# Kernel tuning notes

Hardware: AMD Instinct MI355X
Metric: run time of the kernel (lower is better)

The kernel has to match this reference:

```python
import jax, jax.numpy as jnp
import numpy as np

RADII = [2, 4]
EPS = 1e-6


def _avg_pool_hw(t, k):
    # valid avg-pool with kernel k, stride 1 over the last two dims
    nd = t.ndim
    win = (1,) * (nd - 2) + (k, k)
    s = jax.lax.reduce_window(t, 0.0, jax.lax.add, win, (1,) * nd, 'VALID')
    return s / float(k * k)


def _patch_cca(x, y, r):
    B, C1, H, W = x.shape
    C2 = y.shape[1]
    k = 2 * r + 1
    pad = ((0, 0), (0, 0), (r, r), (r, r))
    xp = jnp.pad(x, pad, mode='reflect')  # (B,C1,Hp,Wp)
    yp = jnp.pad(y, pad, mode='reflect')  # (B,C2,Hp,Wp)

    # local second moments via outer products + avg pooling
    xx = _avg_pool_hw(xp[:, :, None] * xp[:, None], k)  # (B,C1,C1,H,W)
    yy = _avg_pool_hw(yp[:, :, None] * yp[:, None], k)  # (B,C2,C2,H,W)
    xy = _avg_pool_hw(xp[:, :, None] * yp[:, None], k)  # (B,C1,C2,H,W)
    xm = _avg_pool_hw(xp, k)  # (B,C1,H,W)
    ym = _avg_pool_hw(yp, k)  # (B,C2,H,W)

    cxx = xx - xm[:, :, None] * xm[:, None]
    cyy = yy - ym[:, :, None] * ym[:, None]
    cxy = xy - xm[:, :, None] * ym[:, None]

    # move matrix dims last: (B,H,W,Ci,Cj)
    cxx = jnp.transpose(cxx, (0, 3, 4, 1, 2)) + EPS * jnp.eye(C1, dtype=x.dtype)
    cyy = jnp.transpose(cyy, (0, 3, 4, 1, 2)) + EPS * jnp.eye(C2, dtype=x.dtype)
    cxy = jnp.transpose(cxy, (0, 3, 4, 1, 2))

    lx_inv = jnp.linalg.inv(jnp.linalg.cholesky(cxx))  # (B,H,W,C1,C1)
    ly_inv = jnp.linalg.inv(jnp.linalg.cholesky(cyy))  # (B,H,W,C2,C2)
    corr = jnp.einsum('bhwij,bhwjk,bhwkl->bhwil', lx_inv, cxy, ly_inv)
    diag = jnp.diagonal(corr, axis1=-2, axis2=-1)  # (B,H,W,min(C1,C2))
    sim = jnp.abs(diag).sum(-1) / min(C1, C2)  # (B,H,W)
    return sim[:, None]  # (B,1,H,W)


def setup_inputs() -> dict:
    key = jax.random.key(0)
    kx, ky = jax.random.split(key)
    B, C, H, W = 2, 6, 512, 512
    x = jax.random.normal(kx, (B, C, H, W), dtype=jnp.float32)
    y = jax.random.normal(ky, (B, C, H, W), dtype=jnp.float32)
    return {'x': x, 'y': y}


def reference(x, y):
    # stack per-radius CCA maps on a trailing axis -> (B,1,H,W,len(RADII))
    return jnp.stack([_patch_cca(x, y, r) for r in RADII], axis=-1)
```

## Files before the change

kernel.cpp:

```cpp
#include <hip/hip_runtime.h>
#include <math.h>

typedef float v2f __attribute__((ext_vector_type(2)));
typedef float v4f __attribute__((ext_vector_type(4)));

#define LT(i,j) ((i)*((i)+1)/2 + (j))

__device__ __forceinline__ int reflect512(int i) {
  int a = (i < 0) ? -i : i;
  int b = 1022 - a;
  return (a < b) ? a : b;
}

constexpr int HB  = 520;
constexpr int PS  = 12;
constexpr int RS  = HB * PS;

__global__ __launch_bounds__(256)
void prep_interleave(const float* __restrict__ xg, const float* __restrict__ yg,
                     float* __restrict__ zb) {
  constexpr int H = 512, W = 512, HW = H * W;
  const int idx = blockIdx.x * 256 + threadIdx.x;
  if (idx >= 2 * HB * HB) return;
  const int b  = idx / (HB * HB);
  const int r2 = idx - b * (HB * HB);
  const int hr = r2 / HB;
  const int wc = r2 - hr * HB;
  const int h = reflect512(hr - 4);
  const int w = reflect512(wc - 4);
  const size_t gp = (size_t)b * 6 * HW + (size_t)h * W + w;
  float xv[6], yv[6];
  #pragma unroll
  for (int c = 0; c < 6; ++c) {
    xv[c] = xg[gp + c * HW];
    yv[c] = yg[gp + c * HW];
  }
  float* o = zb + (size_t)idx * PS;
  v4f p0 = {xv[0], xv[1], xv[2], xv[3]};
  v4f p1 = {xv[4], xv[5], yv[0], yv[1]};
  v4f p2 = {yv[2], yv[3], yv[4], yv[5]};
  *(v4f*)(o + 0) = p0;
  *(v4f*)(o + 4) = p1;
  *(v4f*)(o + 8) = p2;
}

__device__ __forceinline__ float gget(const v2f* accd, const v2f* accs,
                                      int a, int b) {
  const int t = LT(a >> 1, b >> 1);
  if (((a & 1) == 0) && ((b & 1) == 0)) return accd[t].x;
  if (((a & 1) == 1) && ((b & 1) == 1)) return accd[t].y;
  if ((a & 1) == 0) return accs[t].x;
  return accs[t].y;
}

__device__ __forceinline__ void cholinv6(float* a) {
  #pragma unroll
  for (int j = 0; j < 6; ++j) {
    float d = a[LT(j,j)];
    #pragma unroll
    for (int p = 0; p < j; ++p) d -= a[LT(j,p)] * a[LT(j,p)];
    const float rd = __builtin_amdgcn_rsqf(d);
    a[LT(j,j)] = rd;
    #pragma unroll
    for (int i = j + 1; i < 6; ++i) {
      float s = a[LT(i,j)];
      #pragma unroll
      for (int p = 0; p < j; ++p) s -= a[LT(i,p)] * a[LT(j,p)];
      a[LT(i,j)] = s * rd;
    }
  }
  #pragma unroll
  for (int j = 0; j < 6; ++j) {
    #pragma unroll
    for (int i = j + 1; i < 6; ++i) {
      float s = 0.0f;
      #pragma unroll
      for (int p = j; p < i; ++p) s += a[LT(i,p)] * a[LT(p,j)];
      a[LT(i,j)] = -s * a[LT(i,i)];
    }
  }
}

template <int K, bool ADD>
__device__ __forceinline__ void row_acc_g(const float* __restrict__ p,
                                          v2f* zs, v2f* accd, v2f* accs) {
  #pragma unroll
  for (int dx = 0; dx < K; ++dx) {
    const v4f l0 = *(const v4f*)(p + dx * PS + 0);
    const v4f l1 = *(const v4f*)(p + dx * PS + 4);
    const v4f l2 = *(const v4f*)(p + dx * PS + 8);
    v2f z[6];
    z[0] = l0.lo; z[1] = l0.hi;
    z[2] = l1.lo; z[3] = l1.hi;
    z[4] = l2.lo; z[5] = l2.hi;
    #pragma unroll
    for (int q = 0; q < 6; ++q) zs[q] = ADD ? (zs[q] + z[q]) : (zs[q] - z[q]);
    int t = 0;
    #pragma unroll
    for (int Kp = 0; Kp < 6; ++Kp) {
      #pragma unroll
      for (int Pp = 0; Pp <= Kp; ++Pp) {
        const v2f c  = z[Pp];
        const v2f cs = __builtin_shufflevector(c, c, 1, 0);
        const v2f a  = ADD ? z[Kp] : -z[Kp];
        accd[t] = __builtin_elementwise_fma(a, c,  accd[t]);
        accs[t] = __builtin_elementwise_fma(a, cs, accs[t]);
        ++t;
      }
    }
  }
}

template <int K>
__device__ __forceinline__ float emit_sim(const v2f* zs, const v2f* accd,
                                          const v2f* accs) {
  constexpr float inv_n = 1.0f / (K * K);
  float mx[6], my[6];
  #pragma unroll
  for (int i = 0; i < 6; ++i) {
    mx[i] = ((i & 1) ? zs[i >> 1].y : zs[i >> 1].x) * inv_n;
    my[i] = ((i & 1) ? zs[3 + (i >> 1)].y : zs[3 + (i >> 1)].x) * inv_n;
  }
  float ax[21];
  {
    int t = 0;
    #pragma unroll
    for (int i = 0; i < 6; ++i)
      #pragma unroll
      for (int j = 0; j <= i; ++j) {
        const float e = (i == j) ? 1e-6f : 0.0f;
        ax[t] = gget(accd, accs, i, j) * inv_n - mx[i] * mx[j] + e;
        ++t;
      }
  }
  cholinv6(ax);
  float ay[21];
  {
    int t = 0;
    #pragma unroll
    for (int i = 0; i < 6; ++i)
      #pragma unroll
      for (int j = 0; j <= i; ++j) {
        const float e = (i == j) ? 1e-6f : 0.0f;
        ay[t] = gget(accd, accs, 6 + i, 6 + j) * inv_n - my[i] * my[j] + e;
        ++t;
      }
  }
  cholinv6(ay);
  float cxy[36];
  #pragma unroll
  for (int i = 0; i < 6; ++i)
    #pragma unroll
    for (int j = 0; j < 6; ++j)
      cxy[i * 6 + j] = fmaf(-mx[i], my[j], gget(accd, accs, 6 + j, i) * inv_n);
  float sim = 0.0f;
  #pragma unroll
  for (int i = 0; i < 6; ++i) {
    float di = 0.0f;
    #pragma unroll
    for (int j = 0; j <= i; ++j) {
      float inner = 0.0f;
      #pragma unroll
      for (int k = i; k < 6; ++k) inner += cxy[j * 6 + k] * ay[LT(k, i)];
      di += ax[LT(i, j)] * inner;
    }
    sim += fabsf(di);
  }
  return sim * (1.0f / 6.0f);
}

template <int R, int V>
__device__ __forceinline__ void run(const float* __restrict__ zb,
                                    float* __restrict__ out, int b, int ri) {
  constexpr int K = 2 * R + 1;
  constexpr int H = 512, W = 512;

  const int h0 = blockIdx.y * (16 * V);
  const int w0 = blockIdx.x * 16;
  const int tx = threadIdx.x & 15;
  const int g  = threadIdx.x >> 4;
  const int hbase = h0 + g * V;
  const int wc = w0 + tx;

  const float* base = zb + (size_t)b * HB * RS
                    + (size_t)(hbase + 4 - R) * RS + (size_t)(wc + 4 - R) * PS;

  v2f zs[6]    = {};
  v2f accd[21] = {};
  v2f accs[21] = {};

  #pragma unroll 1
  for (int dy = 0; dy < K; ++dy)
    row_acc_g<K, true>(base + dy * RS, zs, accd, accs);

  out[((size_t)((b * H + hbase) * W + wc)) * 2 + ri] =
      emit_sim<K>(zs, accd, accs);

  #pragma unroll 1
  for (int s = 1; s < V; ++s) {
    row_acc_g<K, true >(base + (s + 2 * R) * RS, zs, accd, accs);
    row_acc_g<K, false>(base + (s - 1)     * RS, zs, accd, accs);
    out[((size_t)((b * H + hbase + s) * W + wc)) * 2 + ri] =
        emit_sim<K>(zs, accd, accs);
  }
}

__global__ __launch_bounds__(256, 2)
void cca_v8(const float* __restrict__ zb, float* __restrict__ out) {
  const int z = blockIdx.z;
  if (z < 2) run<2, 8>(zb, out, z, 0);
  else       run<4, 8>(zb, out, z - 2, 1);
}

extern "C" void kernel_launch(void* const* d_in, const int* in_sizes, int n_in,
                              void* d_out, int out_size, void* d_ws, size_t ws_size,
                              hipStream_t stream) {
  const float* x = (const float*)d_in[0];
  const float* y = (const float*)d_in[1];
  float* out = (float*)d_out;
  float* zb  = (float*)d_ws;

  {
    const int n = 2 * HB * HB;
    prep_interleave<<<dim3((n + 255) / 256), dim3(256), 0, stream>>>(x, y, zb);
  }
  dim3 grid(512 / 16, 512 / (16 * 8), 4);
  cca_v8<<<grid, dim3(256), 0, stream>>>(zb, out);
}
```

Before: 138.7 us.

## Vectorize prep interleave and rebalance radius work across grid blocks

The prep kernel now has each thread handle four consecutive columns. Interior threads use 128-bit loads, and only the reflected border uses scalar loads. The main kernel grid is rebuilt so the heavier radius-4 path runs with 4 rows per thread over more blocks, while the radius-2 path keeps 8 rows per thread. This is meant to even out per-block work and cut tail imbalance. The cost is more sliding-window restarts for radius 4, plus remapped indexing.

```diff
diff --git a/kernel.cpp b/kernel.cpp
--- a/kernel.cpp
+++ b/kernel.cpp
@@ -17,31 +17,51 @@
 constexpr int RS  = HB * PS;
 
 __global__ __launch_bounds__(256)
-void prep_interleave(const float* __restrict__ xg, const float* __restrict__ yg,
-                     float* __restrict__ zb) {
+void prep_interleave4(const float* __restrict__ xg, const float* __restrict__ yg,
+                      float* __restrict__ zb) {
   constexpr int H = 512, W = 512, HW = H * W;
+  constexpr int WQ = HB / 4;
   const int idx = blockIdx.x * 256 + threadIdx.x;
-  if (idx >= 2 * HB * HB) return;
-  const int b  = idx / (HB * HB);
-  const int r2 = idx - b * (HB * HB);
-  const int hr = r2 / HB;
-  const int wc = r2 - hr * HB;
-  const int h = reflect512(hr - 4);
-  const int w = reflect512(wc - 4);
-  const size_t gp = (size_t)b * 6 * HW + (size_t)h * W + w;
-  float xv[6], yv[6];
-  #pragma unroll
-  for (int c = 0; c < 6; ++c) {
-    xv[c] = xg[gp + c * HW];
-    yv[c] = yg[gp + c * HW];
-  }
-  float* o = zb + (size_t)idx * PS;
-  v4f p0 = {xv[0], xv[1], xv[2], xv[3]};
-  v4f p1 = {xv[4], xv[5], yv[0], yv[1]};
-  v4f p2 = {yv[2], yv[3], yv[4], yv[5]};
-  *(v4f*)(o + 0) = p0;
-  *(v4f*)(o + 4) = p1;
-  *(v4f*)(o + 8) = p2;
+  if (idx >= 2 * HB * WQ) return;
+  const int b  = idx / (HB * WQ);
+  const int r2 = idx - b * (HB * WQ);
+  const int hr = r2 / WQ;
+  const int q  = r2 - hr * WQ;
+  const int h  = reflect512(hr - 4);
+  const int w0 = q * 4 - 4;
+  const size_t rowbase = (size_t)b * 6 * HW + (size_t)h * W;
+
+  float xv[6][4], yv[6][4];
+  if (w0 >= 0 && w0 + 3 < W) {
+    #pragma unroll
+    for (int c = 0; c < 6; ++c) {
+      const v4f vx = *(const v4f*)(xg + rowbase + (size_t)c * HW + w0);
+      const v4f vy = *(const v4f*)(yg + rowbase + (size_t)c * HW + w0);
+      #pragma unroll
+      for (int j = 0; j < 4; ++j) { xv[c][j] = vx[j]; yv[c][j] = vy[j]; }
+    }
+  } else {
+    #pragma unroll
+    for (int j = 0; j < 4; ++j) {
+      const int w = reflect512(w0 + j);
+      #pragma unroll
+      for (int c = 0; c < 6; ++c) {
+        xv[c][j] = xg[rowbase + (size_t)c * HW + w];
+        yv[c][j] = yg[rowbase + (size_t)c * HW + w];
+      }
+    }
+  }
+
+  float* o = zb + ((size_t)(b * HB + hr) * HB + q * 4) * PS;
+  #pragma unroll
+  for (int j = 0; j < 4; ++j) {
+    v4f p0 = {xv[0][j], xv[1][j], xv[2][j], xv[3][j]};
+    v4f p1 = {xv[4][j], xv[5][j], yv[0][j], yv[1][j]};
+    v4f p2 = {yv[2][j], yv[3][j], yv[4][j], yv[5][j]};
+    *(v4f*)(o + j * PS + 0) = p0;
+    *(v4f*)(o + j * PS + 4) = p1;
+    *(v4f*)(o + j * PS + 8) = p2;
+  }
 }
 
 __device__ __forceinline__ float gget(const v2f* accd, const v2f* accs,
@@ -171,11 +191,11 @@
 
 template <int R, int V>
 __device__ __forceinline__ void run(const float* __restrict__ zb,
-                                    float* __restrict__ out, int b, int ri) {
+                                    float* __restrict__ out, int b, int ri,
+                                    int h0) {
   constexpr int K = 2 * R + 1;
   constexpr int H = 512, W = 512;
 
-  const int h0 = blockIdx.y * (16 * V);
   const int w0 = blockIdx.x * 16;
   const int tx = threadIdx.x & 15;
   const int g  = threadIdx.x >> 4;
@@ -206,10 +226,14 @@
 }
 
 __global__ __launch_bounds__(256, 2)
-void cca_v8(const float* __restrict__ zb, float* __restrict__ out) {
+void cca_bal(const float* __restrict__ zb, float* __restrict__ out) {
   const int z = blockIdx.z;
-  if (z < 2) run<2, 8>(zb, out, z, 0);
-  else       run<4, 8>(zb, out, z - 2, 1);
+  if (z < 2) {
+    run<4, 4>(zb, out, z, 1, (int)blockIdx.y * (16 * 4));
+  } else {
+    const int b = (int)(blockIdx.y >> 2);
+    run<2, 8>(zb, out, b, 0, (int)(blockIdx.y & 3) * (16 * 8));
+  }
 }
 
 extern "C" void kernel_launch(void* const* d_in, const int* in_sizes, int n_in,
@@ -221,9 +245,9 @@
   float* zb  = (float*)d_ws;
 
   {
-    const int n = 2 * HB * HB;
-    prep_interleave<<<dim3((n + 255) / 256), dim3(256), 0, stream>>>(x, y, zb);
-  }
-  dim3 grid(512 / 16, 512 / (16 * 8), 4);
-  cca_v8<<<grid, dim3(256), 0, stream>>>(zb, out);
-}
+    const int n = 2 * HB * (HB / 4);
+    prep_interleave4<<<dim3((n + 255) / 256), dim3(256), 0, stream>>>(x, y, zb);
+  }
+  dim3 grid(512 / 16, 8, 3);
+  cca_bal<<<grid, dim3(256), 0, stream>>>(zb, out);
+}
```

Measured after the change: 151.5 us. 1.09x slower.
